# Performance work log

Measured on AMD Instinct MI355X. Metric: run time of the kernel, lower is better.

Reference implementation:

```python
import jax, jax.numpy as jnp
import numpy as np

DIM = 768
H = 12        # query heads
HKV = 4       # kv heads
G = H // HKV  # GQA group size
HD = 64       # head dim
CAP = 50.0    # soft cap (Gemma-2 style)
EPS = 1e-6
SCALE = HD ** -0.5
B, T, S = 1, 128, 256


def setup_inputs() -> dict:
    key = jax.random.key(0)
    ks = jax.random.split(key, 5)
    s = DIM ** -0.5
    x = jax.random.normal(ks[0], (B, T, S, DIM), jnp.float32)
    Wq = jax.random.normal(ks[1], (DIM, H * HD), jnp.float32) * s
    Wk = jax.random.normal(ks[2], (DIM, HKV * HD), jnp.float32) * s
    Wv = jax.random.normal(ks[3], (DIM, HKV * HD), jnp.float32) * s
    Wo = jax.random.normal(ks[4], (H * HD, DIM), jnp.float32) * s
    q_norm_w = jnp.ones((HD,), jnp.float32)
    k_norm_w = jnp.ones((HD,), jnp.float32)
    return {"x": x, "Wq": Wq, "Wk": Wk, "Wv": Wv, "Wo": Wo,
            "q_norm_w": q_norm_w, "k_norm_w": k_norm_w}


def _rmsnorm(x, w):
    # x: (..., HD)
    return x * jax.lax.rsqrt(jnp.mean(x * x, axis=-1, keepdims=True) + EPS) * w


def reference(x, Wq, Wk, Wv, Wo, q_norm_w, k_norm_w):
    b, t, s, d = x.shape
    n = b * s
    # fold spatial into batch: temporal attention per spatial position
    xf = x.transpose(0, 2, 1, 3).reshape(n, t, d)             # (N, T, D)
    q = (xf @ Wq).reshape(n, t, H, HD).transpose(0, 2, 1, 3)   # (N, H, T, hd)
    k = (xf @ Wk).reshape(n, t, HKV, HD).transpose(0, 2, 1, 3) # (N, Hkv, T, hd)
    v = (xf @ Wv).reshape(n, t, HKV, HD).transpose(0, 2, 1, 3)
    # QKNorm (per-head RMSNorm on head_dim)
    q = _rmsnorm(q, q_norm_w)
    k = _rmsnorm(k, k_norm_w)
    # GQA without materializing repeated K/V: split q heads into (Hkv, G)
    # (repeat_interleave maps query head h -> kv head h // G, matching kv*G+g)
    qg = q.reshape(n, HKV, G, t, HD)
    attn = jnp.einsum('bkgtd,bksd->bkgts', qg, k) * SCALE      # (N, Hkv, G, T, T)
    attn = CAP * jnp.tanh(attn / CAP)                          # soft cap
    causal = jnp.triu(jnp.ones((t, t), bool), 1)               # True above diag
    attn = jnp.where(causal, -jnp.inf, attn)
    attn = jax.nn.softmax(attn, axis=-1)
    out = jnp.einsum('bkgts,bksd->bkgtd', attn, v)             # (N, Hkv, G, T, hd)
    out = out.reshape(n, H, t, HD).transpose(0, 2, 1, 3).reshape(n, t, H * HD)
    out = out @ Wo                                             # (N, T, D)
    return out.reshape(b, s, t, d).transpose(0, 2, 1, 3)        # (B, T, S, D)
```

## Files before the change

### kernel.cpp

```cpp
#include <hip/hip_runtime.h>
#include <stdint.h>
#include <stddef.h>

#define DIM 768
#define NH  12
#define NKV 4
#define HD  64
#define TT  128
#define NS  256

typedef __attribute__((ext_vector_type(8))) short bf16x8;
typedef __attribute__((ext_vector_type(4))) float f32x4;
typedef __attribute__((ext_vector_type(4))) unsigned int u32x4;
typedef __attribute__((ext_vector_type(2))) unsigned int u32x2;

__device__ __forceinline__ unsigned short f2bf(float f) {
  union { float f; unsigned int u; } v; v.f = f;
  return (unsigned short)((v.u + 0x7FFFu + ((v.u >> 16) & 1u)) >> 16);
}

__device__ __forceinline__ void gload_lds16(const void* g, void* l) {
  __builtin_amdgcn_global_load_lds(
      (const __attribute__((address_space(1))) unsigned int*)g,
      (__attribute__((address_space(3))) unsigned int*)l, 16, 0, 0);
}

__global__ __launch_bounds__(256)
void prep_kernel(const float* __restrict__ x, const float* __restrict__ Wq,
                 const float* __restrict__ Wk, const float* __restrict__ Wv,
                 const float* __restrict__ Wo, unsigned short* __restrict__ Wt,
                 unsigned short* __restrict__ WoT, unsigned short* __restrict__ xb) {
  const int b = blockIdx.x, tid = threadIdx.x;
  if (b < 6144) {
    int idx = b * 256 + tid;
    const int n1 = 1280 * DIM;
    if (idx < n1) {
      int c = idx / DIM, kk = idx - c * DIM;
      float v;
      if (c < 768)       v = Wq[kk * 768 + c];
      else if (c < 1024) v = Wk[kk * 256 + (c - 768)];
      else               v = Wv[kk * 256 + (c - 1024)];
      Wt[idx] = f2bf(v);
    } else {
      int i2 = idx - n1;
      int c = i2 / DIM, kk = i2 - c * DIM;
      WoT[i2] = f2bf(Wo[kk * 768 + c]);
    }
  } else {
    int g = (b - 6144) * 256 + tid;
    int r = g / 192;
    int k = g - r * 192;
    int t = r >> 8, n = r & 255;
    f32x4 f = *reinterpret_cast<const f32x4*>(x + (size_t)g * 4);
    u32x2 pk;
    pk[0] = (unsigned)f2bf(f[0]) | ((unsigned)f2bf(f[1]) << 16);
    pk[1] = (unsigned)f2bf(f[2]) | ((unsigned)f2bf(f[3]) << 16);
    *reinterpret_cast<u32x2*>(xb + (size_t)((n << 7) + t) * DIM + k * 4) = pk;
  }
}


#define STAGE_A(bufp, ko)                                                    \
  { unsigned short* Ad = lds + (bufp) * 24576;                               \
    gload_lds16(asrc + (size_t)(wave * 8) * DIM + (ko), Ad + (wave * 8) * 64);\
    gload_lds16(asrc + (size_t)(64 + wave * 8) * DIM + (ko), Ad + (64 + wave * 8) * 64); }
#define STAGE_B01(bufp, ko)                                                  \
  { unsigned short* Bd = lds + (bufp) * 24576 + 8192;                        \
    gload_lds16(bsrc + (size_t)(wave * 8) * DIM + (ko), Bd + (wave * 8) * 64);\
    gload_lds16(bsrc + (size_t)(64 + wave * 8) * DIM + (ko), Bd + (64 + wave * 8) * 64); }
#define STAGE_B23(bufp, ko)                                                  \
  { unsigned short* Bd = lds + (bufp) * 24576 + 8192;                        \
    gload_lds16(bsrc + (size_t)(128 + wave * 8) * DIM + (ko), Bd + (128 + wave * 8) * 64);\
    gload_lds16(bsrc + (size_t)(192 + wave * 8) * DIM + (ko), Bd + (192 + wave * 8) * 64); }

#define LDA(ks, m) (*(const bf16x8*)(Ab + (wmw * 64 + (m) * 16 + cl) * 128 + (((ks) * 64 + rowg * 16) ^ swzr)))
#define LDB(ks, n) (*(const bf16x8*)(Bb + (wn * 64 + (n) * 16 + cl) * 128 + (((ks) * 64 + rowg * 16) ^ swzr)))

#define MFMA8(mlo, av0, av1)                                                 \
  __builtin_amdgcn_s_setprio(1);                                             \
  _Pragma("unroll")                                                          \
  for (int nn = 0; nn < 4; ++nn) {                                           \
    acc[(mlo)][nn]     = __builtin_amdgcn_mfma_f32_16x16x32_bf16(av0, bb[nn], acc[(mlo)][nn], 0, 0, 0);     \
    acc[(mlo) + 1][nn] = __builtin_amdgcn_mfma_f32_16x16x32_bf16(av1, bb[nn], acc[(mlo) + 1][nn], 0, 0, 0); \
  }                                                                          \
  __builtin_amdgcn_s_setprio(0);

#define KLOOP_8PHASE                                                         \
  STAGE_A(0, 0); STAGE_B01(0, 0); STAGE_B23(0, 0);                           \
  STAGE_A(1, 64); STAGE_B01(1, 64); STAGE_B23(1, 64);                        \
  asm volatile("s_waitcnt vmcnt(6)" ::: "memory");                           \
  __builtin_amdgcn_s_barrier();                                              \
  _Pragma("unroll")                                                          \
  for (int kt = 0; kt < 12; ++kt) {                                          \
    const char* Ab = (const char*)(lds + (kt % 3) * 24576);                  \
    const char* Bb = Ab + 16384;                                             \
    const int bufn = (kt + 2) % 3; const int kon = (kt + 2) * 64;            \
    bf16x8 a0, a1, bb[4];                                                    \
                                                     \
    a0 = LDA(0, 0); a1 = LDA(0, 1);                                          \
    bb[0] = LDB(0, 0); bb[1] = LDB(0, 1); bb[2] = LDB(0, 2); bb[3] = LDB(0, 3);\
    if (kt < 10) STAGE_A(bufn, kon);                                         \
    __builtin_amdgcn_s_barrier();                                            \
    asm volatile("s_waitcnt lgkmcnt(0)" ::: "memory");                       \
    MFMA8(0, a0, a1);                                                        \
    __builtin_amdgcn_s_barrier();                                            \
                                                     \
    a0 = LDA(0, 2); a1 = LDA(0, 3);                                          \
    if (kt < 10) STAGE_B01(bufn, kon);                                       \
    __builtin_amdgcn_s_barrier();                                            \
    asm volatile("s_waitcnt lgkmcnt(0)" ::: "memory");                       \
    MFMA8(2, a0, a1);                                                        \
    __builtin_amdgcn_s_barrier();                                            \
                                                     \
    a0 = LDA(1, 0); a1 = LDA(1, 1);                                          \
    bb[0] = LDB(1, 0); bb[1] = LDB(1, 1); bb[2] = LDB(1, 2); bb[3] = LDB(1, 3);\
    if (kt < 10) STAGE_B23(bufn, kon);                                       \
    __builtin_amdgcn_s_barrier();                                            \
    asm volatile("s_waitcnt lgkmcnt(0)" ::: "memory");                       \
    MFMA8(0, a0, a1);                                                        \
    __builtin_amdgcn_s_barrier();                                            \
                                    \
    a0 = LDA(1, 2); a1 = LDA(1, 3);                                          \
    if (kt <= 9) { asm volatile("s_waitcnt vmcnt(6)" ::: "memory"); }        \
    else         { asm volatile("s_waitcnt vmcnt(0)" ::: "memory"); }        \
    __builtin_amdgcn_s_barrier();                                            \
    asm volatile("s_waitcnt lgkmcnt(0)" ::: "memory");                       \
    MFMA8(2, a0, a1);                                                        \
    __builtin_amdgcn_s_barrier();                                            \
  }

__global__ __launch_bounds__(512, 2)
void qkv_kernel(const unsigned short* __restrict__ xb, const float* __restrict__ qnw,
                const float* __restrict__ knw, const unsigned short* __restrict__ Wt,
                unsigned short* __restrict__ qb, unsigned short* __restrict__ kb,
                unsigned short* __restrict__ vTb) {
  extern __shared__ unsigned short lds[];
  const int b = blockIdx.x;
  const int x8 = b & 7, idx = b >> 3;
  const int cbt = idx % 5;
  const int n   = (idx / 5) * 8 + x8;
  const int tid = threadIdx.x;
  const int wave = tid >> 6, lane = tid & 63;
  const int cl = lane & 15, rowg = lane >> 4;
  const int wmw = wave >> 2, wn = wave & 3;
  const int l8 = lane >> 3, s8 = lane & 7;
  const unsigned short* asrc = xb + (size_t)(n * TT + l8) * DIM + (s8 ^ l8) * 8;
  const unsigned short* bsrc = Wt + (size_t)(cbt * 256 + l8) * DIM + (s8 ^ l8) * 8;
  const int swzr = (cl & 7) << 4;
  f32x4 acc[4][4] = {};

  KLOOP_8PHASE;

  __syncthreads();

  if (cbt == 4) {
    const int kv = wn;
    unsigned short* dst = vTb + (size_t)((n * NKV + kv) * HD) * TT;
    #pragma unroll
    for (int m = 0; m < 4; ++m) {
      const int tb = wmw * 64 + m * 16 + rowg * 4;
      #pragma unroll
      for (int nn = 0; nn < 4; ++nn) {
        const int d = nn * 16 + cl;
        u32x2 pk;
        pk[0] = (unsigned)f2bf(acc[m][nn][0]) | ((unsigned)f2bf(acc[m][nn][1]) << 16);
        pk[1] = (unsigned)f2bf(acc[m][nn][2]) | ((unsigned)f2bf(acc[m][nn][3]) << 16);
        *reinterpret_cast<u32x2*>(dst + (size_t)d * TT + tb) = pk;
      }
    }
  } else {
    const int isq = (cbt < 3);
    const float* nw = isq ? qnw : knw;
    float wfrag[4];
    #pragma unroll
    for (int nn = 0; nn < 4; ++nn) wfrag[nn] = nw[nn * 16 + cl];
    const float rs = isq ? 0.125f : 1.0f;
    #pragma unroll
    for (int m = 0; m < 4; ++m) {
      #pragma unroll
      for (int j = 0; j < 4; ++j) {
        const int t = wmw * 64 + m * 16 + rowg * 4 + j;
        float ss = 0.f;
        #pragma unroll
        for (int nn = 0; nn < 4; ++nn) { float v = acc[m][nn][j]; ss += v * v; }
        #pragma unroll
        for (int dlt = 1; dlt < 16; dlt <<= 1) ss += __shfl_xor(ss, dlt);
        const float r = rsqrtf(ss * (1.f / 64.f) + 1e-6f) * rs;
        #pragma unroll
        for (int nn = 0; nn < 4; ++nn)
          lds[wn * 8192 + t * 64 + nn * 16 + cl] = f2bf(acc[m][nn][j] * r * wfrag[nn]);
      }
    }
    __syncthreads();
    unsigned short* gdst = isq ? qb + ((size_t)n * NH + cbt * 4) * TT * HD
                               : kb + (size_t)n * NKV * TT * HD;
    #pragma unroll
    for (int i = 0; i < 8; ++i) {
      const int c = tid + 512 * i;
      *reinterpret_cast<u32x4*>(gdst + c * 8) = *reinterpret_cast<const u32x4*>(lds + c * 8);
    }
  }
}

__global__ __launch_bounds__(256)
void attn_kernel(const unsigned short* __restrict__ qb, const unsigned short* __restrict__ kb,
                 const unsigned short* __restrict__ vTb, unsigned short* __restrict__ ab) {
  extern __shared__ char smem[];
  unsigned short (*Ks)[72]   = reinterpret_cast<unsigned short (*)[72]>(smem);
  unsigned short (*Vts)[136] = reinterpret_cast<unsigned short (*)[136]>(smem + 18432);
  unsigned short (*Pl)[136]  = reinterpret_cast<unsigned short (*)[136]>(smem + 35840);
  const int b = blockIdx.x;
  const int x8 = b & 7, idx = b >> 3;
  const int kv = idx & 3;
  const int n  = (idx >> 2) * 8 + x8;
  const int tid = threadIdx.x, wave = tid >> 6, lane = tid & 63;
  const int cl = lane & 15, rowg = lane >> 4;

  const unsigned short* ksrc = kb + (size_t)(n * NKV + kv) * TT * HD;
  const unsigned short* vsrc = vTb + (size_t)(n * NKV + kv) * HD * TT;
  #pragma unroll
  for (int i = 0; i < 4; ++i) {
    int c = tid + 256 * i, r = c >> 3, seg = c & 7;
    *reinterpret_cast<u32x4*>(&Ks[r][seg * 8]) = *reinterpret_cast<const u32x4*>(ksrc + c * 8);
  }
  #pragma unroll
  for (int i = 0; i < 4; ++i) {
    int c = tid + 256 * i, r = c >> 4, seg = c & 15;
    *reinterpret_cast<u32x4*>(&Vts[r][seg * 8]) = *reinterpret_cast<const u32x4*>(vsrc + c * 8);
  }
  __syncthreads();

  for (int hh = 0; hh < 3; ++hh) {
    const int h = kv * 3 + hh;
    const unsigned short* qsrc = qb + (size_t)(n * NH + h) * TT * HD;
    f32x4 sc[2][8] = {};
    #pragma unroll
    for (int ks = 0; ks < 2; ++ks) {
      bf16x8 a[2], bbf[8];
      #pragma unroll
      for (int m = 0; m < 2; ++m)
        a[m] = *reinterpret_cast<const bf16x8*>(
            qsrc + (size_t)(wave * 32 + m * 16 + cl) * HD + ks * 32 + rowg * 8);
      #pragma unroll
      for (int nn = 0; nn < 8; ++nn)
        bbf[nn] = *reinterpret_cast<const bf16x8*>(&Ks[nn * 16 + cl][ks * 32 + rowg * 8]);
      #pragma unroll
      for (int m = 0; m < 2; ++m)
        #pragma unroll
        for (int nn = 0; nn < 8; ++nn)
          sc[m][nn] = __builtin_amdgcn_mfma_f32_16x16x32_bf16(a[m], bbf[nn], sc[m][nn], 0, 0, 0);
    }
    #pragma unroll
    for (int m = 0; m < 2; ++m) {
      #pragma unroll
      for (int j = 0; j < 4; ++j) {
        const int rowv = wave * 32 + m * 16 + rowg * 4 + j;
        float mx = -__builtin_inff();
        #pragma unroll
        for (int nn = 0; nn < 8; ++nn) {
          float s = sc[m][nn][j];
          float e = __expf(s * 0.04f);
          s = 50.f - 100.f * __builtin_amdgcn_rcpf(e + 1.f);
          if (nn * 16 + cl > rowv) s = -__builtin_inff();
          sc[m][nn][j] = s;
          mx = fmaxf(mx, s);
        }
        #pragma unroll
        for (int d = 1; d < 16; d <<= 1) mx = fmaxf(mx, __shfl_xor(mx, d));
        float sum = 0.f;
        #pragma unroll
        for (int nn = 0; nn < 8; ++nn) {
          float e = __expf(sc[m][nn][j] - mx);
          sc[m][nn][j] = e;
          sum += e;
        }
        #pragma unroll
        for (int d = 1; d < 16; d <<= 1) sum += __shfl_xor(sum, d);
        const float inv = __builtin_amdgcn_rcpf(sum);
        #pragma unroll
        for (int nn = 0; nn < 8; ++nn)
          Pl[rowv][nn * 16 + cl] = f2bf(sc[m][nn][j] * inv);
      }
    }
    __syncthreads();
    f32x4 o[2][4] = {};
    #pragma unroll
    for (int ks = 0; ks < 4; ++ks) {
      bf16x8 a[2], bbf[4];
      #pragma unroll
      for (int m = 0; m < 2; ++m)
        a[m] = *reinterpret_cast<const bf16x8*>(&Pl[wave * 32 + m * 16 + cl][ks * 32 + rowg * 8]);
      #pragma unroll
      for (int nn = 0; nn < 4; ++nn)
        bbf[nn] = *reinterpret_cast<const bf16x8*>(&Vts[nn * 16 + cl][ks * 32 + rowg * 8]);
      #pragma unroll
      for (int m = 0; m < 2; ++m)
        #pragma unroll
        for (int nn = 0; nn < 4; ++nn)
          o[m][nn] = __builtin_amdgcn_mfma_f32_16x16x32_bf16(a[m], bbf[nn], o[m][nn], 0, 0, 0);
    }
    unsigned short* dst = ab + (size_t)n * TT * DIM + h * HD;
    #pragma unroll
    for (int m = 0; m < 2; ++m)
      #pragma unroll
      for (int j = 0; j < 4; ++j) {
        int t = wave * 32 + m * 16 + rowg * 4 + j;
        #pragma unroll
        for (int nn = 0; nn < 4; ++nn)
          dst[(size_t)t * DIM + nn * 16 + cl] = f2bf(o[m][nn][j]);
      }
    __syncthreads();
  }
}

__global__ __launch_bounds__(512, 2)
void out_kernel(const unsigned short* __restrict__ ab, const unsigned short* __restrict__ WoT,
                float* __restrict__ out) {
  extern __shared__ unsigned short lds[];
  const int b = blockIdx.x;
  const int x8 = b & 7, idx = b >> 3;
  const int cbt = idx % 3;
  const int n   = (idx / 3) * 8 + x8;
  const int tid = threadIdx.x;
  const int wave = tid >> 6, lane = tid & 63;
  const int cl = lane & 15, rowg = lane >> 4;
  const int wmw = wave >> 2, wn = wave & 3;
  const int l8 = lane >> 3, s8 = lane & 7;
  const unsigned short* asrc = ab  + (size_t)(n * TT + l8) * DIM + (s8 ^ l8) * 8;
  const unsigned short* bsrc = WoT + (size_t)(cbt * 256 + l8) * DIM + (s8 ^ l8) * 8;
  const int swzr = (cl & 7) << 4;
  f32x4 acc[4][4] = {};

  KLOOP_8PHASE;

  #pragma unroll
  for (int m = 0; m < 4; ++m)
    #pragma unroll
    for (int j = 0; j < 4; ++j) {
      int t = wmw * 64 + m * 16 + rowg * 4 + j;
      #pragma unroll
      for (int nn = 0; nn < 4; ++nn)
        out[(size_t)(t * NS + n) * DIM + cbt * 256 + wn * 64 + nn * 16 + cl] = acc[m][nn][j];
    }
}

extern "C" void kernel_launch(void* const* d_in, const int* in_sizes, int n_in,
                              void* d_out, int out_size, void* d_ws, size_t ws_size,
                              hipStream_t stream) {
  const float* x   = (const float*)d_in[0];
  const float* Wq  = (const float*)d_in[1];
  const float* Wk  = (const float*)d_in[2];
  const float* Wv  = (const float*)d_in[3];
  const float* Wo  = (const float*)d_in[4];
  const float* qnw = (const float*)d_in[5];
  const float* knw = (const float*)d_in[6];
  (void)in_sizes; (void)n_in; (void)out_size;

  char* ws = (char*)d_ws;
  unsigned short* Wt  = (unsigned short*)(ws + 0);
  unsigned short* WoT = (unsigned short*)(ws + 1966080);
  unsigned short* qb  = (unsigned short*)(ws + 3145728);
  unsigned short* kb  = (unsigned short*)(ws + 53477376);
  unsigned short* vTb = (unsigned short*)(ws + 70254592);
  unsigned short* ab  = (unsigned short*)(ws + 87031808);
  unsigned short* xb  = ab;
  if (ws_size < 137363456) return;

  hipFuncSetAttribute(reinterpret_cast<const void*>(qkv_kernel),
                      hipFuncAttributeMaxDynamicSharedMemorySize, 147456);
  hipFuncSetAttribute(reinterpret_cast<const void*>(out_kernel),
                      hipFuncAttributeMaxDynamicSharedMemorySize, 147456);
  hipFuncSetAttribute(reinterpret_cast<const void*>(attn_kernel),
                      hipFuncAttributeMaxDynamicSharedMemorySize, 70656);

  prep_kernel<<<30720, 256, 0, stream>>>(x, Wq, Wk, Wv, Wo, Wt, WoT, xb);
  qkv_kernel<<<1280, 512, 147456, stream>>>(xb, qnw, knw, Wt, qb, kb, vTb);
  attn_kernel<<<1024, 256, 70656, stream>>>(qb, kb, vTb, ab);
  out_kernel<<<768, 512, 147456, stream>>>(ab, WoT, (float*)d_out);
}
```

Baseline: 225.5 us.

## Enlarge GEMM tiles to 256x256 with simple double-buffered K loop

The QKV and output GEMM kernels now compute two spatial positions (256 rows) per block instead of one, so each staged weight tile is reused twice and the grids shrink to 640 and 384 blocks. The 3-stage 8-phase interleaved pipeline is replaced by a plain 2-buffer loop with one __syncthreads per K step, each wave holding 8x4 accumulators. This cuts weight traffic and barrier count, but it raises register pressure (128 accumulator floats per lane), loses the fine-grained overlap of loads with MFMA, and the smaller grid may fill the CUs poorly. 128KB of LDS per block likely limits each CU to one block.

New measurement: 230.8 us. +2.4%, slower.

```diff
diff --git a/kernel.cpp b/kernel.cpp
--- a/kernel.cpp
+++ b/kernel.cpp
@@ -60,73 +60,43 @@
 }
 
 
-#define STAGE_A(bufp, ko)                                                    \
-  { unsigned short* Ad = lds + (bufp) * 24576;                               \
-    gload_lds16(asrc + (size_t)(wave * 8) * DIM + (ko), Ad + (wave * 8) * 64);\
-    gload_lds16(asrc + (size_t)(64 + wave * 8) * DIM + (ko), Ad + (64 + wave * 8) * 64); }
-#define STAGE_B01(bufp, ko)                                                  \
-  { unsigned short* Bd = lds + (bufp) * 24576 + 8192;                        \
-    gload_lds16(bsrc + (size_t)(wave * 8) * DIM + (ko), Bd + (wave * 8) * 64);\
-    gload_lds16(bsrc + (size_t)(64 + wave * 8) * DIM + (ko), Bd + (64 + wave * 8) * 64); }
-#define STAGE_B23(bufp, ko)                                                  \
-  { unsigned short* Bd = lds + (bufp) * 24576 + 8192;                        \
+#define STAGE256(bufp, ko)                                                       \
+  { unsigned short* Ad = lds + (bufp) * 32768;                                   \
+    unsigned short* Bd = Ad + 16384;                                             \
+    gload_lds16(a0src + (size_t)(wave * 8) * DIM + (ko), Ad + (wave * 8) * 64);  \
+    gload_lds16(a0src + (size_t)(64 + wave * 8) * DIM + (ko), Ad + (64 + wave * 8) * 64); \
+    gload_lds16(a1src + (size_t)(wave * 8) * DIM + (ko), Ad + (128 + wave * 8) * 64);     \
+    gload_lds16(a1src + (size_t)(64 + wave * 8) * DIM + (ko), Ad + (192 + wave * 8) * 64);\
+    gload_lds16(bsrc + (size_t)(wave * 8) * DIM + (ko), Bd + (wave * 8) * 64);   \
+    gload_lds16(bsrc + (size_t)(64 + wave * 8) * DIM + (ko), Bd + (64 + wave * 8) * 64);  \
     gload_lds16(bsrc + (size_t)(128 + wave * 8) * DIM + (ko), Bd + (128 + wave * 8) * 64);\
     gload_lds16(bsrc + (size_t)(192 + wave * 8) * DIM + (ko), Bd + (192 + wave * 8) * 64); }
 
-#define LDA(ks, m) (*(const bf16x8*)(Ab + (wmw * 64 + (m) * 16 + cl) * 128 + (((ks) * 64 + rowg * 16) ^ swzr)))
-#define LDB(ks, n) (*(const bf16x8*)(Bb + (wn * 64 + (n) * 16 + cl) * 128 + (((ks) * 64 + rowg * 16) ^ swzr)))
-
-#define MFMA8(mlo, av0, av1)                                                 \
-  __builtin_amdgcn_s_setprio(1);                                             \
-  _Pragma("unroll")                                                          \
-  for (int nn = 0; nn < 4; ++nn) {                                           \
-    acc[(mlo)][nn]     = __builtin_amdgcn_mfma_f32_16x16x32_bf16(av0, bb[nn], acc[(mlo)][nn], 0, 0, 0);     \
-    acc[(mlo) + 1][nn] = __builtin_amdgcn_mfma_f32_16x16x32_bf16(av1, bb[nn], acc[(mlo) + 1][nn], 0, 0, 0); \
-  }                                                                          \
-  __builtin_amdgcn_s_setprio(0);
-
-#define KLOOP_8PHASE                                                         \
-  STAGE_A(0, 0); STAGE_B01(0, 0); STAGE_B23(0, 0);                           \
-  STAGE_A(1, 64); STAGE_B01(1, 64); STAGE_B23(1, 64);                        \
-  asm volatile("s_waitcnt vmcnt(6)" ::: "memory");                           \
-  __builtin_amdgcn_s_barrier();                                              \
-  _Pragma("unroll")                                                          \
-  for (int kt = 0; kt < 12; ++kt) {                                          \
-    const char* Ab = (const char*)(lds + (kt % 3) * 24576);                  \
-    const char* Bb = Ab + 16384;                                             \
-    const int bufn = (kt + 2) % 3; const int kon = (kt + 2) * 64;            \
-    bf16x8 a0, a1, bb[4];                                                    \
-                                                     \
-    a0 = LDA(0, 0); a1 = LDA(0, 1);                                          \
-    bb[0] = LDB(0, 0); bb[1] = LDB(0, 1); bb[2] = LDB(0, 2); bb[3] = LDB(0, 3);\
-    if (kt < 10) STAGE_A(bufn, kon);                                         \
-    __builtin_amdgcn_s_barrier();                                            \
-    asm volatile("s_waitcnt lgkmcnt(0)" ::: "memory");                       \
-    MFMA8(0, a0, a1);                                                        \
-    __builtin_amdgcn_s_barrier();                                            \
-                                                     \
-    a0 = LDA(0, 2); a1 = LDA(0, 3);                                          \
-    if (kt < 10) STAGE_B01(bufn, kon);                                       \
-    __builtin_amdgcn_s_barrier();                                            \
-    asm volatile("s_waitcnt lgkmcnt(0)" ::: "memory");                       \
-    MFMA8(2, a0, a1);                                                        \
-    __builtin_amdgcn_s_barrier();                                            \
-                                                     \
-    a0 = LDA(1, 0); a1 = LDA(1, 1);                                          \
-    bb[0] = LDB(1, 0); bb[1] = LDB(1, 1); bb[2] = LDB(1, 2); bb[3] = LDB(1, 3);\
-    if (kt < 10) STAGE_B23(bufn, kon);                                       \
-    __builtin_amdgcn_s_barrier();                                            \
-    asm volatile("s_waitcnt lgkmcnt(0)" ::: "memory");                       \
-    MFMA8(0, a0, a1);                                                        \
-    __builtin_amdgcn_s_barrier();                                            \
-                                    \
-    a0 = LDA(1, 2); a1 = LDA(1, 3);                                          \
-    if (kt <= 9) { asm volatile("s_waitcnt vmcnt(6)" ::: "memory"); }        \
-    else         { asm volatile("s_waitcnt vmcnt(0)" ::: "memory"); }        \
-    __builtin_amdgcn_s_barrier();                                            \
-    asm volatile("s_waitcnt lgkmcnt(0)" ::: "memory");                       \
-    MFMA8(2, a0, a1);                                                        \
-    __builtin_amdgcn_s_barrier();                                            \
+#define KLOOP256                                                                 \
+  STAGE256(0, 0);                                                                \
+  __syncthreads();                                                               \
+  for (int kt = 0; kt < 12; ++kt) {                                              \
+    if (kt < 11) STAGE256((kt + 1) & 1, (kt + 1) * 64);                          \
+    const char* Ab = (const char*)(lds + (kt & 1) * 32768);                      \
+    const char* Bb = Ab + 32768;                                                 \
+    _Pragma("unroll")                                                            \
+    for (int ks = 0; ks < 2; ++ks) {                                             \
+      bf16x8 a[8], bbf[4];                                                       \
+      _Pragma("unroll")                                                          \
+      for (int m = 0; m < 8; ++m)                                                \
+        a[m] = *(const bf16x8*)(Ab + (wmw * 128 + m * 16 + cl) * 128 + ((ks * 64 + rowg * 16) ^ swzr)); \
+      _Pragma("unroll")                                                          \
+      for (int nn = 0; nn < 4; ++nn)                                             \
+        bbf[nn] = *(const bf16x8*)(Bb + (wn * 64 + nn * 16 + cl) * 128 + ((ks * 64 + rowg * 16) ^ swzr)); \
+      __builtin_amdgcn_s_setprio(1);                                             \
+      _Pragma("unroll")                                                          \
+      for (int m = 0; m < 8; ++m)                                                \
+        _Pragma("unroll")                                                        \
+        for (int nn = 0; nn < 4; ++nn)                                           \
+          acc[m][nn] = __builtin_amdgcn_mfma_f32_16x16x32_bf16(a[m], bbf[nn], acc[m][nn], 0, 0, 0); \
+      __builtin_amdgcn_s_setprio(0);                                             \
+    }                                                                            \
+    __syncthreads();                                                             \
   }
 
 __global__ __launch_bounds__(512, 2)
@@ -138,27 +108,30 @@
   const int b = blockIdx.x;
   const int x8 = b & 7, idx = b >> 3;
   const int cbt = idx % 5;
-  const int n   = (idx / 5) * 8 + x8;
+  const int np  = (idx / 5) * 8 + x8;
+  const int n0  = np * 2;
   const int tid = threadIdx.x;
   const int wave = tid >> 6, lane = tid & 63;
   const int cl = lane & 15, rowg = lane >> 4;
   const int wmw = wave >> 2, wn = wave & 3;
   const int l8 = lane >> 3, s8 = lane & 7;
-  const unsigned short* asrc = xb + (size_t)(n * TT + l8) * DIM + (s8 ^ l8) * 8;
-  const unsigned short* bsrc = Wt + (size_t)(cbt * 256 + l8) * DIM + (s8 ^ l8) * 8;
+  const int segs = (s8 ^ l8) * 8;
+  const unsigned short* a0src = xb + (size_t)(n0 * TT + l8) * DIM + segs;
+  const unsigned short* a1src = xb + (size_t)((n0 + 1) * TT + l8) * DIM + segs;
+  const unsigned short* bsrc  = Wt + (size_t)(cbt * 256 + l8) * DIM + segs;
   const int swzr = (cl & 7) << 4;
-  f32x4 acc[4][4] = {};
-
-  KLOOP_8PHASE;
+  f32x4 acc[8][4] = {};
+
+  KLOOP256;
 
   __syncthreads();
+  const int n = n0 + wmw;
 
   if (cbt == 4) {
-    const int kv = wn;
-    unsigned short* dst = vTb + (size_t)((n * NKV + kv) * HD) * TT;
-    #pragma unroll
-    for (int m = 0; m < 4; ++m) {
-      const int tb = wmw * 64 + m * 16 + rowg * 4;
+    unsigned short* dst = vTb + (size_t)((n * NKV + wn) * HD) * TT;
+    #pragma unroll
+    for (int m = 0; m < 8; ++m) {
+      const int tb = m * 16 + rowg * 4;
       #pragma unroll
       for (int nn = 0; nn < 4; ++nn) {
         const int d = nn * 16 + cl;
@@ -175,11 +148,12 @@
     #pragma unroll
     for (int nn = 0; nn < 4; ++nn) wfrag[nn] = nw[nn * 16 + cl];
     const float rs = isq ? 0.125f : 1.0f;
-    #pragma unroll
-    for (int m = 0; m < 4; ++m) {
+    unsigned short* slab = lds + (wmw * 4 + wn) * 8192;
+    #pragma unroll
+    for (int m = 0; m < 8; ++m) {
       #pragma unroll
       for (int j = 0; j < 4; ++j) {
-        const int t = wmw * 64 + m * 16 + rowg * 4 + j;
+        const int t = m * 16 + rowg * 4 + j;
         float ss = 0.f;
         #pragma unroll
         for (int nn = 0; nn < 4; ++nn) { float v = acc[m][nn][j]; ss += v * v; }
@@ -188,16 +162,21 @@
         const float r = rsqrtf(ss * (1.f / 64.f) + 1e-6f) * rs;
         #pragma unroll
         for (int nn = 0; nn < 4; ++nn)
-          lds[wn * 8192 + t * 64 + nn * 16 + cl] = f2bf(acc[m][nn][j] * r * wfrag[nn]);
+          slab[t * 64 + nn * 16 + cl] = f2bf(acc[m][nn][j] * r * wfrag[nn]);
       }
     }
     __syncthreads();
-    unsigned short* gdst = isq ? qb + ((size_t)n * NH + cbt * 4) * TT * HD
-                               : kb + (size_t)n * NKV * TT * HD;
-    #pragma unroll
-    for (int i = 0; i < 8; ++i) {
+    #pragma unroll
+    for (int i = 0; i < 16; ++i) {
       const int c = tid + 512 * i;
-      *reinterpret_cast<u32x4*>(gdst + c * 8) = *reinterpret_cast<const u32x4*>(lds + c * 8);
+      const int s = c >> 10, within = c & 1023;
+      const int nn2 = n0 + (s >> 2);
+      size_t off;
+      if (isq) off = ((size_t)nn2 * NH + cbt * 4 + (s & 3)) * TT * HD;
+      else     off = ((size_t)nn2 * NKV + (s & 3)) * TT * HD;
+      unsigned short* gdst = (isq ? qb : kb) + off + within * 8;
+      *reinterpret_cast<u32x4*>(gdst) =
+          *reinterpret_cast<const u32x4*>(lds + (size_t)s * 8192 + within * 8);
     }
   }
 }
@@ -320,24 +299,28 @@
   const int b = blockIdx.x;
   const int x8 = b & 7, idx = b >> 3;
   const int cbt = idx % 3;
-  const int n   = (idx / 3) * 8 + x8;
+  const int np  = (idx / 3) * 8 + x8;
+  const int n0  = np * 2;
   const int tid = threadIdx.x;
   const int wave = tid >> 6, lane = tid & 63;
   const int cl = lane & 15, rowg = lane >> 4;
   const int wmw = wave >> 2, wn = wave & 3;
   const int l8 = lane >> 3, s8 = lane & 7;
-  const unsigned short* asrc = ab  + (size_t)(n * TT + l8) * DIM + (s8 ^ l8) * 8;
-  const unsigned short* bsrc = WoT + (size_t)(cbt * 256 + l8) * DIM + (s8 ^ l8) * 8;
+  const int segs = (s8 ^ l8) * 8;
+  const unsigned short* a0src = ab + (size_t)(n0 * TT + l8) * DIM + segs;
+  const unsigned short* a1src = ab + (size_t)((n0 + 1) * TT + l8) * DIM + segs;
+  const unsigned short* bsrc  = WoT + (size_t)(cbt * 256 + l8) * DIM + segs;
   const int swzr = (cl & 7) << 4;
-  f32x4 acc[4][4] = {};
-
-  KLOOP_8PHASE;
-
+  f32x4 acc[8][4] = {};
+
+  KLOOP256;
+
+  const int n = n0 + wmw;
   #pragma unroll
-  for (int m = 0; m < 4; ++m)
+  for (int m = 0; m < 8; ++m)
     #pragma unroll
     for (int j = 0; j < 4; ++j) {
-      int t = wmw * 64 + m * 16 + rowg * 4 + j;
+      const int t = m * 16 + rowg * 4 + j;
       #pragma unroll
       for (int nn = 0; nn < 4; ++nn)
         out[(size_t)(t * NS + n) * DIM + cbt * 256 + wn * 64 + nn * 16 + cl] = acc[m][nn][j];
@@ -367,14 +350,14 @@
   if (ws_size < 137363456) return;
 
   hipFuncSetAttribute(reinterpret_cast<const void*>(qkv_kernel),
-                      hipFuncAttributeMaxDynamicSharedMemorySize, 147456);
+                      hipFuncAttributeMaxDynamicSharedMemorySize, 131072);
   hipFuncSetAttribute(reinterpret_cast<const void*>(out_kernel),
-                      hipFuncAttributeMaxDynamicSharedMemorySize, 147456);
+                      hipFuncAttributeMaxDynamicSharedMemorySize, 131072);
   hipFuncSetAttribute(reinterpret_cast<const void*>(attn_kernel),
                       hipFuncAttributeMaxDynamicSharedMemorySize, 70656);
 
   prep_kernel<<<30720, 256, 0, stream>>>(x, Wq, Wk, Wv, Wo, Wt, WoT, xb);
-  qkv_kernel<<<1280, 512, 147456, stream>>>(xb, qnw, knw, Wt, qb, kb, vTb);
+  qkv_kernel<<<640, 512, 131072, stream>>>(xb, qnw, knw, Wt, qb, kb, vTb);
   attn_kernel<<<1024, 256, 70656, stream>>>(qb, kb, vTb, ab);
-  out_kernel<<<768, 512, 147456, stream>>>(ab, WoT, (float*)d_out);
-}
+  out_kernel<<<384, 512, 131072, stream>>>(ab, WoT, (float*)d_out);
+}
```
